# Kernel tuning notes

Measured on AMD Instinct MI355X. Metric: run time of the kernel, lower is better.

Reference implementation:

```python
import jax, jax.numpy as jnp
import numpy as np

N = 100000      # nodes
E = 1600000     # edges
D_IN = 16       # input_dim
D_H = 32        # hidden_dim
D_OUT = 1       # output_dim
N_ITERS = 2
D_CAT = D_H + D_IN          # node feature after cat([H, X])
D_EDGE = 2 * D_CAT          # edge MLP input dim


def setup_inputs() -> dict:
    key = jax.random.key(0)
    ks = jax.random.split(key, 10)
    x = jax.random.normal(ks[0], (N, D_IN), jnp.float32)
    edge_index = jax.random.randint(ks[1], (2, E), 0, N, dtype=jnp.int32)
    # inputnet: Linear(D_IN -> D_H) + Tanh
    W_in = jax.random.normal(ks[2], (D_H, D_IN), jnp.float32) / np.sqrt(D_IN)
    b_in = jnp.zeros((D_H,), jnp.float32)
    # convnn (EdgeConv nn): Linear(D_EDGE -> D_H) + Sigmoid
    W_c = jax.random.normal(ks[3], (D_H, D_EDGE), jnp.float32) / np.sqrt(D_EDGE)
    b_c = jnp.zeros((D_H,), jnp.float32)
    # outputnet: Linear(D_H -> D_OUT) + Sigmoid
    W_out = jax.random.normal(ks[4], (D_OUT, D_H), jnp.float32) / np.sqrt(D_H)
    b_out = jnp.zeros((D_OUT,), jnp.float32)
    return {"x": x, "edge_index": edge_index, "W_in": W_in, "b_in": b_in,
            "W_c": W_c, "b_c": b_c, "W_out": W_out, "b_out": b_out}


def reference(x, edge_index, W_in, b_in, W_c, b_c, W_out, b_out):
    src = edge_index[0]  # x_j (source / neighbor)
    dst = edge_index[1]  # x_i (target, aggregation index)

    H = jnp.tanh(x @ W_in.T + b_in)            # [N, D_H]
    feats = jnp.concatenate([H, x], axis=-1)    # [N, D_CAT]

    for _ in range(N_ITERS):
        xi = feats[dst]                          # [E, D_CAT] gather targets
        xj = feats[src]                          # [E, D_CAT] gather sources
        # PyG EdgeConv message: nn(cat([x_i, x_j - x_i]))
        msg = jax.nn.sigmoid(
            jnp.concatenate([xi, xj - xi], axis=-1) @ W_c.T + b_c)  # [E, D_H]
        H = jax.ops.segment_sum(msg, dst, num_segments=N)           # aggr='add'
        feats = jnp.concatenate([H, x], axis=-1)

    sum_H = jnp.mean(H, axis=0)                  # [D_H]
    return jax.nn.sigmoid(sum_H @ W_out.T + b_out)  # [D_OUT]
```

## Files before the change

kernel.cpp:

```cpp
#include <hip/hip_runtime.h>

#define D_H 32
#define NREP 32
#define SLOTS 48
#define BIN_SHIFT 8
#define MAXNB 512
#define BIN_CAP 5120
#define SB 256
#define NPB 64


__device__ __forceinline__ void conv_and_flush(
        float st[48][NPB + 1], const float* __restrict__ W_c,
        const float* __restrict__ b_c, float* __restrict__ A, float* __restrict__ B,
        int N, int n0, int tid, int nl, int qq) {
    float f[48];
#pragma unroll
    for (int i = 0; i < 48; ++i) f[i] = st[i][nl];
    float pr[8], br[8];
#pragma unroll 2
    for (int jj = 0; jj < 8; ++jj) {
        int j = qq * 8 + jj;
        const float* w = W_c + j * 96;
        float p = b_c[j];
        float bb = 0.f;
#pragma unroll
        for (int i = 0; i < 48; ++i) {
            p  += f[i] * w[i];
            bb += f[i] * w[48 + i];
        }
        pr[jj] = p - bb;
        br[jj] = bb;
    }
    __syncthreads();
#pragma unroll
    for (int jj = 0; jj < 8; ++jj) st[qq * 8 + jj][nl] = pr[jj];
    __syncthreads();
    float4* A4 = (float4*)(A + (size_t)n0 * D_H);
#pragma unroll
    for (int k = 0; k < 2; ++k) {
        int i4 = k * 256 + tid;
        int nn = i4 >> 3;
        int j0 = (i4 & 7) * 4;
        if (n0 + nn < N) {
            float4 v = {st[j0][nn], st[j0 + 1][nn], st[j0 + 2][nn], st[j0 + 3][nn]};
            A4[i4] = v;
        }
    }
    __syncthreads();
#pragma unroll
    for (int jj = 0; jj < 8; ++jj) st[qq * 8 + jj][nl] = br[jj];
    __syncthreads();
    float4* B4 = (float4*)(B + (size_t)n0 * D_H);
#pragma unroll
    for (int k = 0; k < 2; ++k) {
        int i4 = k * 256 + tid;
        int nn = i4 >> 3;
        int j0 = (i4 & 7) * 4;
        if (n0 + nn < N) {
            float4 v = {st[j0][nn], st[j0 + 1][nn], st[j0 + 2][nn], st[j0 + 3][nn]};
            B4[i4] = v;
        }
    }
}

__global__ __launch_bounds__(256) void k_ab0(const float* __restrict__ x,
                      const float* __restrict__ W_in, const float* __restrict__ b_in,
                      const float* __restrict__ W_c, const float* __restrict__ b_c,
                      float* __restrict__ A, float* __restrict__ B, int N) {
    __shared__ float st[48][NPB + 1];
    int tid = threadIdx.x;
    int n0 = blockIdx.x * NPB;
    int nl = tid & (NPB - 1);
    int qq = tid >> 6;
    {
        int row = tid >> 2, c = tid & 3;
        float4 v = {0.f, 0.f, 0.f, 0.f};
        if (n0 + row < N) v = ((const float4*)(x + (size_t)(n0 + row) * 16))[c];
        st[32 + 4 * c + 0][row] = v.x;
        st[32 + 4 * c + 1][row] = v.y;
        st[32 + 4 * c + 2][row] = v.z;
        st[32 + 4 * c + 3][row] = v.w;
    }
    __syncthreads();
    {
        float xf[16];
#pragma unroll
        for (int i = 0; i < 16; ++i) xf[i] = st[32 + i][nl];
#pragma unroll
        for (int jj = 0; jj < 8; ++jj) {
            int j = qq * 8 + jj;
            const float* w = W_in + j * 16;
            float acc = b_in[j];
#pragma unroll
            for (int i = 0; i < 16; ++i) acc += xf[i] * w[i];
            st[j][nl] = tanhf(acc);
        }
    }
    __syncthreads();
    conv_and_flush(st, W_c, b_c, A, B, N, n0, tid, nl, qq);
}

__global__ __launch_bounds__(256) void k_ab1(const float* __restrict__ H,
                      const float* __restrict__ x, const float* __restrict__ W_c,
                      const float* __restrict__ b_c, float* __restrict__ A,
                      float* __restrict__ B, int N) {
    __shared__ float st[48][NPB + 1];
    int tid = threadIdx.x;
    int n0 = blockIdx.x * NPB;
    int nl = tid & (NPB - 1);
    int qq = tid >> 6;
#pragma unroll
    for (int k = 0; k < 2; ++k) {
        int i = k * 256 + tid;
        int row = i >> 3, c = i & 7;
        float4 v = {0.f, 0.f, 0.f, 0.f};
        if (n0 + row < N) v = ((const float4*)(H + (size_t)(n0 + row) * D_H))[c];
        st[4 * c + 0][row] = v.x;
        st[4 * c + 1][row] = v.y;
        st[4 * c + 2][row] = v.z;
        st[4 * c + 3][row] = v.w;
    }
    {
        int row = tid >> 2, c = tid & 3;
        float4 v = {0.f, 0.f, 0.f, 0.f};
        if (n0 + row < N) v = ((const float4*)(x + (size_t)(n0 + row) * 16))[c];
        st[32 + 4 * c + 0][row] = v.x;
        st[32 + 4 * c + 1][row] = v.y;
        st[32 + 4 * c + 2][row] = v.z;
        st[32 + 4 * c + 3][row] = v.w;
    }
    __syncthreads();
    conv_and_flush(st, W_c, b_c, A, B, N, n0, tid, nl, qq);
}

__global__ __launch_bounds__(256) void k_bin(const int* __restrict__ src,
                                             const int* __restrict__ dst,
                                             int* __restrict__ binCnt,
                                             unsigned int* __restrict__ ebuf, int E) {
    __shared__ int hist[MAXNB];
    int tid = threadIdx.x;
    for (int i = tid; i < MAXNB; i += 256) hist[i] = 0;
    __syncthreads();
    int chunk = (E + SB - 1) / SB;
    int lo = blockIdx.x * chunk;
    int hi = lo + chunk; if (hi > E) hi = E;
    for (int e = lo + tid; e < hi; e += 256) {
        int b = dst[e] >> BIN_SHIFT;
        atomicAdd(&hist[b], 1);
    }
    __syncthreads();
    for (int b = tid; b < MAXNB; b += 256) {
        int c = hist[b];
        int base = c ? atomicAdd(&binCnt[b], c) : 0;
        hist[b] = b * BIN_CAP + base;
    }
    __syncthreads();
    for (int e = lo + tid; e < hi; e += 256) {
        int d = dst[e];
        int s = src[e];
        int b = d >> BIN_SHIFT;
        int pos = atomicAdd(&hist[b], 1);
        if ((unsigned)(pos - b * BIN_CAP) < (unsigned)BIN_CAP)
            ebuf[pos] = ((unsigned)(d & 255) << 24) | (unsigned)s;
    }
}

__global__ __launch_bounds__(256) void k_place(const int* __restrict__ binCnt,
                                               const unsigned int* __restrict__ ebuf,
                                               int* __restrict__ ssrcp,
                                               int* __restrict__ cntG, int N) {
    __shared__ int cnt[256];
    int tid = threadIdx.x;
    int w = blockIdx.x;
    cnt[tid] = 0;
    __syncthreads();
    int n = binCnt[w]; if (n > BIN_CAP) n = BIN_CAP;
    int base = w * BIN_CAP;
    for (int j = tid; j < n; j += 256) {
        unsigned int v = ebuf[base + j];
        int ld = v >> 24;
        int s = v & 0xFFFFFF;
        int slot = atomicAdd(&cnt[ld], 1);
        if (slot < SLOTS)
            ssrcp[(size_t)((w << BIN_SHIFT) + ld) * SLOTS + slot] = s;
    }
    __syncthreads();
    int node = (w << BIN_SHIFT) + tid;
    if (node < N) cntG[node] = cnt[tid] < SLOTS ? cnt[tid] : SLOTS;
}


__global__ void k_gather1(const int* __restrict__ cntG, const int* __restrict__ ssrcp,
                          const float* __restrict__ A, const float* __restrict__ B,
                          float* __restrict__ H, int N) {
    int t = blockIdx.x * blockDim.x + threadIdx.x;
    int d = t >> 5;
    if (d >= N) return;
    int l = t & 31;
    int q = l & 7;
    int s = l >> 3;
    int len = cntG[d];
    const int* base = ssrcp + (size_t)d * SLOTS;
    float4 a4 = ((const float4*)(A + (size_t)d * D_H))[q];
    float4 acc = {0.f, 0.f, 0.f, 0.f};
    int j = s;
    for (; j + 4 < len; j += 8) {
        int s0 = base[j], s1 = base[j + 4];
        float4 b0 = ((const float4*)(B + (size_t)s0 * D_H))[q];
        float4 b1 = ((const float4*)(B + (size_t)s1 * D_H))[q];
        acc.x += 1.f / (1.f + __expf(-(a4.x + b0.x)));
        acc.y += 1.f / (1.f + __expf(-(a4.y + b0.y)));
        acc.z += 1.f / (1.f + __expf(-(a4.z + b0.z)));
        acc.w += 1.f / (1.f + __expf(-(a4.w + b0.w)));
        acc.x += 1.f / (1.f + __expf(-(a4.x + b1.x)));
        acc.y += 1.f / (1.f + __expf(-(a4.y + b1.y)));
        acc.z += 1.f / (1.f + __expf(-(a4.z + b1.z)));
        acc.w += 1.f / (1.f + __expf(-(a4.w + b1.w)));
    }
    if (j < len) {
        int s0 = base[j];
        float4 b0 = ((const float4*)(B + (size_t)s0 * D_H))[q];
        acc.x += 1.f / (1.f + __expf(-(a4.x + b0.x)));
        acc.y += 1.f / (1.f + __expf(-(a4.y + b0.y)));
        acc.z += 1.f / (1.f + __expf(-(a4.z + b0.z)));
        acc.w += 1.f / (1.f + __expf(-(a4.w + b0.w)));
    }
    acc.x += __shfl_xor(acc.x, 8);  acc.y += __shfl_xor(acc.y, 8);
    acc.z += __shfl_xor(acc.z, 8);  acc.w += __shfl_xor(acc.w, 8);
    acc.x += __shfl_xor(acc.x, 16); acc.y += __shfl_xor(acc.y, 16);
    acc.z += __shfl_xor(acc.z, 16); acc.w += __shfl_xor(acc.w, 16);
    if (s == 0) ((float4*)(H + (size_t)d * D_H))[q] = acc;
}

__global__ void k_gather2(const int* __restrict__ cntG, const int* __restrict__ ssrcp,
                          const float* __restrict__ A, const float* __restrict__ B,
                          float* __restrict__ Srep, int N) {
    int l = threadIdx.x & 31;
    int slot = threadIdx.x >> 5;
    int q = l & 7;
    int s = l >> 3;
    int d = blockIdx.x * 8 + slot;
    float4 acc = {0.f, 0.f, 0.f, 0.f};
    if (d < N) {
        int len = cntG[d];
        const int* base = ssrcp + (size_t)d * SLOTS;
        float4 a4 = ((const float4*)(A + (size_t)d * D_H))[q];
        int j = s;
        for (; j + 4 < len; j += 8) {
            int s0 = base[j], s1 = base[j + 4];
            float4 b0 = ((const float4*)(B + (size_t)s0 * D_H))[q];
            float4 b1 = ((const float4*)(B + (size_t)s1 * D_H))[q];
            acc.x += 1.f / (1.f + __expf(-(a4.x + b0.x)));
            acc.y += 1.f / (1.f + __expf(-(a4.y + b0.y)));
            acc.z += 1.f / (1.f + __expf(-(a4.z + b0.z)));
            acc.w += 1.f / (1.f + __expf(-(a4.w + b0.w)));
            acc.x += 1.f / (1.f + __expf(-(a4.x + b1.x)));
            acc.y += 1.f / (1.f + __expf(-(a4.y + b1.y)));
            acc.z += 1.f / (1.f + __expf(-(a4.z + b1.z)));
            acc.w += 1.f / (1.f + __expf(-(a4.w + b1.w)));
        }
        if (j < len) {
            int s0 = base[j];
            float4 b0 = ((const float4*)(B + (size_t)s0 * D_H))[q];
            acc.x += 1.f / (1.f + __expf(-(a4.x + b0.x)));
            acc.y += 1.f / (1.f + __expf(-(a4.y + b0.y)));
            acc.z += 1.f / (1.f + __expf(-(a4.z + b0.z)));
            acc.w += 1.f / (1.f + __expf(-(a4.w + b0.w)));
        }
    }
    acc.x += __shfl_xor(acc.x, 8);  acc.y += __shfl_xor(acc.y, 8);
    acc.z += __shfl_xor(acc.z, 8);  acc.w += __shfl_xor(acc.w, 8);
    acc.x += __shfl_xor(acc.x, 16); acc.y += __shfl_xor(acc.y, 16);
    acc.z += __shfl_xor(acc.z, 16); acc.w += __shfl_xor(acc.w, 16);
    __shared__ float red[8][32];
    if (s == 0) {
        red[slot][4 * q + 0] = acc.x;
        red[slot][4 * q + 1] = acc.y;
        red[slot][4 * q + 2] = acc.z;
        red[slot][4 * q + 3] = acc.w;
    }
    __syncthreads();
    if (threadIdx.x < 32) {
        float sm = 0.f;
#pragma unroll
        for (int r = 0; r < 8; ++r) sm += red[r][threadIdx.x];
        unsafeAtomicAdd(&Srep[(blockIdx.x & (NREP - 1)) * D_H + threadIdx.x], sm);
    }
}

__global__ void k_final(const float* __restrict__ Srep, const float* __restrict__ W_out,
                        const float* __restrict__ b_out, float* __restrict__ out,
                        float invN) {
    int j = threadIdx.x;
    float v = 0.f;
    if (j < 32) {
        float s = 0.f;
#pragma unroll
        for (int r = 0; r < NREP; ++r) s += Srep[r * D_H + j];
        v = s * invN * W_out[j];
    }
#pragma unroll
    for (int off = 32; off > 0; off >>= 1) v += __shfl_down(v, off);
    if (j == 0) out[0] = 1.f / (1.f + __expf(-(v + b_out[0])));
}

extern "C" void kernel_launch(void* const* d_in, const int* in_sizes, int n_in,
                              void* d_out, int out_size, void* d_ws, size_t ws_size,
                              hipStream_t stream) {
    const float* x     = (const float*)d_in[0];
    const int*   ei    = (const int*)d_in[1];
    const float* W_in  = (const float*)d_in[2];
    const float* b_in  = (const float*)d_in[3];
    const float* W_c   = (const float*)d_in[4];
    const float* b_c   = (const float*)d_in[5];
    const float* W_out = (const float*)d_in[6];
    const float* b_out = (const float*)d_in[7];

    const int N = in_sizes[0] / 16;
    const int E = in_sizes[1] / 2;
    const int* src = ei;
    const int* dst = ei + E;

    const int NB = (N + 255) >> BIN_SHIFT;

    float* H    = (float*)d_ws;
    float* A    = H + (size_t)N * D_H;
    float* B    = A + (size_t)N * D_H;
    float* Srep = B + (size_t)N * D_H;
    int*   cntG   = (int*)(Srep + NREP * D_H);
    int*   binCnt = cntG + N;
    int*   ssrcp  = binCnt + MAXNB;
    unsigned int* ebuf = (unsigned int*)H;

    float* out = (float*)d_out;

    const int abBlocks = (N + NPB - 1) / NPB;

    hipMemsetAsync(binCnt, 0, MAXNB * sizeof(int), stream);
    k_bin<<<SB, 256, 0, stream>>>(src, dst, binCnt, ebuf, E);
    k_place<<<NB, 256, 0, stream>>>(binCnt, ebuf, ssrcp, cntG, N);

    k_ab0<<<abBlocks, 256, 0, stream>>>(x, W_in, b_in, W_c, b_c, A, B, N);
    k_gather1<<<(int)(((size_t)N * 32 + 255) / 256), 256, 0, stream>>>(cntG, ssrcp, A, B, H, N);

    k_ab1<<<abBlocks, 256, 0, stream>>>(H, x, W_c, b_c, A, B, N);
    hipMemsetAsync(Srep, 0, NREP * D_H * sizeof(float), stream);
    k_gather2<<<(N + 7) / 8, 256, 0, stream>>>(cntG, ssrcp, A, B, Srep, N);

    k_final<<<1, 64, 0, stream>>>(Srep, W_out, b_out, out, 1.f / (float)N);
}
```

Baseline: 291.9 us.

## Remap per-node linear kernels to lane-per-output with register-resident weights

Rewrites k_ab0 and k_ab1 so each lane owns one output channel j and holds its row of W_c (and W_in) in registers. Node features sit row-major in shared memory and are read as broadcast float4s. A and B are written directly with coalesced stores instead of going through transposed shared-memory staging with extra barriers. This removes the repeated global/constant weight loads and the transpose-and-flush syncs, at the cost of about 112 extra registers per thread, which may lower occupancy.

```diff
diff --git a/kernel.cpp b/kernel.cpp
--- a/kernel.cpp
+++ b/kernel.cpp
@@ -7,131 +7,132 @@
 #define MAXNB 512
 #define BIN_CAP 5120
 #define SB 256
-#define NPB 64
-
-
-__device__ __forceinline__ void conv_and_flush(
-        float st[48][NPB + 1], const float* __restrict__ W_c,
-        const float* __restrict__ b_c, float* __restrict__ A, float* __restrict__ B,
-        int N, int n0, int tid, int nl, int qq) {
-    float f[48];
-#pragma unroll
-    for (int i = 0; i < 48; ++i) f[i] = st[i][nl];
-    float pr[8], br[8];
-#pragma unroll 2
-    for (int jj = 0; jj < 8; ++jj) {
-        int j = qq * 8 + jj;
-        const float* w = W_c + j * 96;
-        float p = b_c[j];
-        float bb = 0.f;
-#pragma unroll
-        for (int i = 0; i < 48; ++i) {
-            p  += f[i] * w[i];
-            bb += f[i] * w[48 + i];
-        }
-        pr[jj] = p - bb;
-        br[jj] = bb;
-    }
-    __syncthreads();
-#pragma unroll
-    for (int jj = 0; jj < 8; ++jj) st[qq * 8 + jj][nl] = pr[jj];
-    __syncthreads();
-    float4* A4 = (float4*)(A + (size_t)n0 * D_H);
-#pragma unroll
-    for (int k = 0; k < 2; ++k) {
-        int i4 = k * 256 + tid;
-        int nn = i4 >> 3;
-        int j0 = (i4 & 7) * 4;
-        if (n0 + nn < N) {
-            float4 v = {st[j0][nn], st[j0 + 1][nn], st[j0 + 2][nn], st[j0 + 3][nn]};
-            A4[i4] = v;
-        }
-    }
-    __syncthreads();
-#pragma unroll
-    for (int jj = 0; jj < 8; ++jj) st[qq * 8 + jj][nl] = br[jj];
-    __syncthreads();
-    float4* B4 = (float4*)(B + (size_t)n0 * D_H);
-#pragma unroll
-    for (int k = 0; k < 2; ++k) {
-        int i4 = k * 256 + tid;
-        int nn = i4 >> 3;
-        int j0 = (i4 & 7) * 4;
-        if (n0 + nn < N) {
-            float4 v = {st[j0][nn], st[j0 + 1][nn], st[j0 + 2][nn], st[j0 + 3][nn]};
-            B4[i4] = v;
-        }
-    }
-}
+#define PNPB 64
+#define SF 52
+
 
 __global__ __launch_bounds__(256) void k_ab0(const float* __restrict__ x,
                       const float* __restrict__ W_in, const float* __restrict__ b_in,
                       const float* __restrict__ W_c, const float* __restrict__ b_c,
                       float* __restrict__ A, float* __restrict__ B, int N) {
-    __shared__ float st[48][NPB + 1];
+    __shared__ float f[PNPB][SF];
     int tid = threadIdx.x;
-    int n0 = blockIdx.x * NPB;
-    int nl = tid & (NPB - 1);
-    int qq = tid >> 6;
+    int n0 = blockIdx.x * PNPB;
+    int wv = tid >> 6;
+    int h  = (tid >> 5) & 1;
+    int j  = tid & 31;
+    float wc[96];
+    {
+        const float4* wr = (const float4*)(W_c + j * 96);
+#pragma unroll
+        for (int q = 0; q < 24; ++q) {
+            float4 v = wr[q];
+            wc[4 * q] = v.x; wc[4 * q + 1] = v.y; wc[4 * q + 2] = v.z; wc[4 * q + 3] = v.w;
+        }
+    }
+    float win[16];
+    {
+        const float4* wr = (const float4*)(W_in + j * 16);
+#pragma unroll
+        for (int q = 0; q < 4; ++q) {
+            float4 v = wr[q];
+            win[4 * q] = v.x; win[4 * q + 1] = v.y; win[4 * q + 2] = v.z; win[4 * q + 3] = v.w;
+        }
+    }
+    float bc = b_c[j];
+    float bi = b_in[j];
     {
         int row = tid >> 2, c = tid & 3;
         float4 v = {0.f, 0.f, 0.f, 0.f};
         if (n0 + row < N) v = ((const float4*)(x + (size_t)(n0 + row) * 16))[c];
-        st[32 + 4 * c + 0][row] = v.x;
-        st[32 + 4 * c + 1][row] = v.y;
-        st[32 + 4 * c + 2][row] = v.z;
-        st[32 + 4 * c + 3][row] = v.w;
-    }
-    __syncthreads();
-    {
-        float xf[16];
-#pragma unroll
-        for (int i = 0; i < 16; ++i) xf[i] = st[32 + i][nl];
-#pragma unroll
-        for (int jj = 0; jj < 8; ++jj) {
-            int j = qq * 8 + jj;
-            const float* w = W_in + j * 16;
-            float acc = b_in[j];
-#pragma unroll
-            for (int i = 0; i < 16; ++i) acc += xf[i] * w[i];
-            st[j][nl] = tanhf(acc);
-        }
-    }
-    __syncthreads();
-    conv_and_flush(st, W_c, b_c, A, B, N, n0, tid, nl, qq);
+        *(float4*)&f[row][32 + 4 * c] = v;
+    }
+    __syncthreads();
+#pragma unroll 2
+    for (int it = 0; it < 8; ++it) {
+        int n = wv * 16 + it * 2 + h;
+        {
+            float4 x0 = *(const float4*)&f[n][32];
+            float4 x1 = *(const float4*)&f[n][36];
+            float4 x2 = *(const float4*)&f[n][40];
+            float4 x3 = *(const float4*)&f[n][44];
+            float acc = bi;
+            acc += x0.x * win[0] + x0.y * win[1] + x0.z * win[2] + x0.w * win[3];
+            acc += x1.x * win[4] + x1.y * win[5] + x1.z * win[6] + x1.w * win[7];
+            acc += x2.x * win[8] + x2.y * win[9] + x2.z * win[10] + x2.w * win[11];
+            acc += x3.x * win[12] + x3.y * win[13] + x3.z * win[14] + x3.w * win[15];
+            f[n][j] = tanhf(acc);
+        }
+        float p = bc, bb = 0.f;
+#pragma unroll
+        for (int q = 0; q < 12; ++q) {
+            float4 v = *(const float4*)&f[n][4 * q];
+            p  += v.x * wc[4 * q]      + v.y * wc[4 * q + 1]
+                + v.z * wc[4 * q + 2]  + v.w * wc[4 * q + 3];
+            bb += v.x * wc[48 + 4 * q]     + v.y * wc[48 + 4 * q + 1]
+                + v.z * wc[48 + 4 * q + 2] + v.w * wc[48 + 4 * q + 3];
+        }
+        int g = n0 + n;
+        if (g < N) {
+            A[(size_t)g * D_H + j] = p - bb;
+            B[(size_t)g * D_H + j] = bb;
+        }
+    }
 }
 
 __global__ __launch_bounds__(256) void k_ab1(const float* __restrict__ H,
                       const float* __restrict__ x, const float* __restrict__ W_c,
                       const float* __restrict__ b_c, float* __restrict__ A,
                       float* __restrict__ B, int N) {
-    __shared__ float st[48][NPB + 1];
+    __shared__ float f[PNPB][SF];
     int tid = threadIdx.x;
-    int n0 = blockIdx.x * NPB;
-    int nl = tid & (NPB - 1);
-    int qq = tid >> 6;
+    int n0 = blockIdx.x * PNPB;
+    int wv = tid >> 6;
+    int h  = (tid >> 5) & 1;
+    int j  = tid & 31;
+    float wc[96];
+    {
+        const float4* wr = (const float4*)(W_c + j * 96);
+#pragma unroll
+        for (int q = 0; q < 24; ++q) {
+            float4 v = wr[q];
+            wc[4 * q] = v.x; wc[4 * q + 1] = v.y; wc[4 * q + 2] = v.z; wc[4 * q + 3] = v.w;
+        }
+    }
+    float bc = b_c[j];
 #pragma unroll
     for (int k = 0; k < 2; ++k) {
         int i = k * 256 + tid;
         int row = i >> 3, c = i & 7;
         float4 v = {0.f, 0.f, 0.f, 0.f};
         if (n0 + row < N) v = ((const float4*)(H + (size_t)(n0 + row) * D_H))[c];
-        st[4 * c + 0][row] = v.x;
-        st[4 * c + 1][row] = v.y;
-        st[4 * c + 2][row] = v.z;
-        st[4 * c + 3][row] = v.w;
+        *(float4*)&f[row][4 * c] = v;
     }
     {
         int row = tid >> 2, c = tid & 3;
         float4 v = {0.f, 0.f, 0.f, 0.f};
         if (n0 + row < N) v = ((const float4*)(x + (size_t)(n0 + row) * 16))[c];
-        st[32 + 4 * c + 0][row] = v.x;
-        st[32 + 4 * c + 1][row] = v.y;
-        st[32 + 4 * c + 2][row] = v.z;
-        st[32 + 4 * c + 3][row] = v.w;
-    }
-    __syncthreads();
-    conv_and_flush(st, W_c, b_c, A, B, N, n0, tid, nl, qq);
+        *(float4*)&f[row][32 + 4 * c] = v;
+    }
+    __syncthreads();
+#pragma unroll 2
+    for (int it = 0; it < 8; ++it) {
+        int n = wv * 16 + it * 2 + h;
+        float p = bc, bb = 0.f;
+#pragma unroll
+        for (int q = 0; q < 12; ++q) {
+            float4 v = *(const float4*)&f[n][4 * q];
+            p  += v.x * wc[4 * q]      + v.y * wc[4 * q + 1]
+                + v.z * wc[4 * q + 2]  + v.w * wc[4 * q + 3];
+            bb += v.x * wc[48 + 4 * q]     + v.y * wc[48 + 4 * q + 1]
+                + v.z * wc[48 + 4 * q + 2] + v.w * wc[48 + 4 * q + 3];
+        }
+        int g = n0 + n;
+        if (g < N) {
+            A[(size_t)g * D_H + j] = p - bb;
+            B[(size_t)g * D_H + j] = bb;
+        }
+    }
 }
 
 __global__ __launch_bounds__(256) void k_bin(const int* __restrict__ src,
@@ -335,7 +336,7 @@
 
     float* out = (float*)d_out;
 
-    const int abBlocks = (N + NPB - 1) / NPB;
+    const int abBlocks = (N + PNPB - 1) / PNPB;
 
     hipMemsetAsync(binCnt, 0, MAXNB * sizeof(int), stream);
     k_bin<<<SB, 256, 0, stream>>>(src, dst, binCnt, ebuf, E);
```

After: 251.6 us. 1.16x faster.
